# Optimization experiments

Hardware: AMD Instinct MI355X
Metric: run time of the kernel (lower is better)

The kernel has to match this reference:

```python
import jax, jax.numpy as jnp
import numpy as np

EPS = 1e-5
B, C, N = 2, 256, 65536


def conv1x1(x, W, b):
    # Conv1d with kernel_size=1: (B,Cin,N) x (Cout,Cin) -> (B,Cout,N)
    return jnp.einsum('oc,bcn->bon', W, x) + b[None, :, None]


def instance_norm(x):
    # InstanceNorm1d, affine=False, biased variance over the spatial dim
    m = jnp.mean(x, axis=-1, keepdims=True)
    v = jnp.var(x, axis=-1, keepdims=True)
    return (x - m) * jax.lax.rsqrt(v + EPS)


def mesh_conv(x, gemm, W, b):
    # MeshCNN MeshConv: gather self + 4 one-ring neighbor edges, symmetric fns, (1,5) conv.
    Bb, Cc, E = x.shape
    xp = jnp.concatenate([jnp.zeros((Bb, Cc, 1), x.dtype), x], axis=2)  # pad slot 0 (for -1/missing)
    eid = jnp.broadcast_to(jnp.arange(E, dtype=gemm.dtype)[None, :, None], (Bb, E, 1))
    Gi = jnp.concatenate([eid, gemm], axis=2) + 1                      # (B,E,5), +1 shift for pad row
    xt = xp.transpose(0, 2, 1)                                          # (B,E+1,C)
    f = jax.vmap(lambda xb, gb: xb[gb])(xt, Gi)                         # (B,E,5,C) gather
    f = f.transpose(0, 3, 1, 2)                                         # (B,C,E,5)
    f0, f1, f2, f3, f4 = (f[..., i] for i in range(5))
    g = jnp.stack([f0, f1 + f3, f2 + f4, jnp.abs(f1 - f3), jnp.abs(f2 - f4)], axis=-1)
    # Conv2d(Cin,Cout,(1,5)) over (B,C,E,5) -> (B,Cout,E)
    return jnp.einsum('ock,bcek->boe', W, g) + b[None, :, None]


def setup_inputs() -> dict:
    key = jax.random.key(0)
    ks = jax.random.split(key, 20)
    s = 0.05
    inp = {
        'x_0': jax.random.normal(ks[0], (B, C, N), jnp.float32),
        'x_1': jax.random.normal(ks[1], (B, C, N), jnp.float32),
        'gemm': jax.random.randint(ks[2], (B, N, 4), 0, N, jnp.int32),
        # conv_a / conv_b: C -> C//4
        'Wa': jax.random.normal(ks[3], (C // 4, C), jnp.float32) * s,
        'ba': jax.random.normal(ks[4], (C // 4,), jnp.float32) * s,
        'Wb': jax.random.normal(ks[5], (C // 4, C), jnp.float32) * s,
        'bb': jax.random.normal(ks[6], (C // 4,), jnp.float32) * s,
        # conv_a_local / conv_b_local: C//2 -> C//2
        'Wal': jax.random.normal(ks[7], (C // 2, C // 2), jnp.float32) * s,
        'bal': jax.random.normal(ks[8], (C // 2,), jnp.float32) * s,
        'Wbl': jax.random.normal(ks[9], (C // 2, C // 2), jnp.float32) * s,
        'bbl': jax.random.normal(ks[10], (C // 2,), jnp.float32) * s,
        # MeshConv weights: (Cout, Cin, 5)
        'Wat': jax.random.normal(ks[11], (C // 2, C // 2, 5), jnp.float32) * s,
        'bat': jax.random.normal(ks[12], (C // 2,), jnp.float32) * s,
        'Wbt': jax.random.normal(ks[13], (C // 2, C // 2, 5), jnp.float32) * s,
        'bbt': jax.random.normal(ks[14], (C // 2,), jnp.float32) * s,
        # fuse convs: C -> C
        'Waf': jax.random.normal(ks[15], (C, C), jnp.float32) * s,
        'baf': jax.random.normal(ks[16], (C,), jnp.float32) * s,
        'Wbf': jax.random.normal(ks[17], (C, C), jnp.float32) * s,
        'bbf': jax.random.normal(ks[18], (C,), jnp.float32) * s,
    }
    return inp


def reference(x_0, x_1, gemm, Wa, ba, Wb, bb, Wal, bal, Wbl, bbl,
              Wat, bat, Wbt, bbt, Waf, baf, Wbf, bbf):
    x_a = conv1x1(x_0, Wa, ba)
    x_b = conv1x1(x_1, Wb, bb)
    x_all = jnp.concatenate([x_a, x_b], axis=1)          # (B, C/2, N)
    a_local = conv1x1(x_all, Wal, bal)
    a_tri = mesh_conv(x_all, gemm, Wat, bat)
    x_a_two = jnp.concatenate([a_local, a_tri], axis=1)  # (B, C, N)
    b_local = conv1x1(x_all, Wbl, bbl)
    b_tri = mesh_conv(x_all, gemm, Wbt, bbt)
    x_b_two = jnp.concatenate([b_local, b_tri], axis=1)
    wa = jax.nn.sigmoid(instance_norm(conv1x1(x_a_two, Waf, baf)))
    wb = jax.nn.sigmoid(instance_norm(conv1x1(x_b_two, Wbf, bbf)))
    w = jax.nn.softmax(jnp.stack([wa, wb], axis=1), axis=1)  # (B,2,C,N)
    return x_0 * w[:, 0] + x_1 * w[:, 1]
```

## Files before the change

### kernel.cpp

```cpp
#include <hip/hip_runtime.h>
#include <stdint.h>

#define NEDGE 65536

typedef __attribute__((ext_vector_type(4))) float f32x4;
typedef __attribute__((ext_vector_type(8))) __bf16 bf16x8;

__device__ __forceinline__ uint16_t f2bf(float f) {
  union { float f; uint32_t u; } v; v.f = f;
  uint32_t r = v.u + 0x7FFFu + ((v.u >> 16) & 1u);
  return (uint16_t)(r >> 16);
}
__device__ __forceinline__ float bflo(uint32_t u) {
  union { uint32_t u; float f; } v; v.u = u << 16; return v.f;
}
__device__ __forceinline__ float bfhi(uint32_t u) {
  union { uint32_t u; float f; } v; v.u = u & 0xFFFF0000u; return v.f;
}
__device__ __forceinline__ uint32_t packbf(float lo, float hi) {
  return (uint32_t)f2bf(lo) | ((uint32_t)f2bf(hi) << 16);
}
__device__ __forceinline__ void gload_lds16(const void* g, void* l) {
  __builtin_amdgcn_global_load_lds(
      (__attribute__((address_space(1))) uint32_t*)(uintptr_t)g,
      (__attribute__((address_space(3))) uint32_t*)l, 16, 0, 0);
}
__device__ __forceinline__ float sigm(float z) { return 1.0f / (1.0f + __expf(-z)); }

__global__ void k_compose(const float* __restrict__ Wal, const float* __restrict__ Wbl,
                          const float* __restrict__ Wat, const float* __restrict__ Wbt,
                          const float* __restrict__ Waf, const float* __restrict__ Wbf,
                          uint16_t* __restrict__ Wt) {
  int id = blockIdx.x * 256 + threadIdx.x;
  if (id >= 512 * 640) return;
  int j = id / 640, kk = id % 640;
  const float* Wf = (j < 256) ? Waf : Wbf;
  const float* Wl = (j < 256) ? Wal : Wbl;
  const float* Wr = (j < 256) ? Wat : Wbt;
  int jj = j & 255;
  float acc = 0.f;
  if (kk < 128) {
    int c = kk;
    for (int o = 0; o < 128; ++o) acc += Wl[o * 128 + c] * Wf[jj * 256 + o];
    for (int o = 0; o < 128; ++o) acc += Wr[(o * 128 + c) * 5 + 0] * Wf[jj * 256 + 128 + o];
  } else {
    int blkid = (kk - 128) >> 7;
    int gk = (blkid == 0) ? 1 : (blkid == 1) ? 3 : (blkid == 2) ? 2 : 4;
    int c = (kk - 128) & 127;
    for (int o = 0; o < 128; ++o) acc += Wr[(o * 128 + c) * 5 + gk] * Wf[jj * 256 + 128 + o];
  }
  Wt[j * 640 + kk] = f2bf(acc);
}

__global__ void k_bias(const float* __restrict__ bal, const float* __restrict__ bat,
                       const float* __restrict__ baf, const float* __restrict__ bbl,
                       const float* __restrict__ bbt, const float* __restrict__ bbf,
                       const float* __restrict__ Waf, const float* __restrict__ Wbf,
                       float* __restrict__ biasF) {
  int id = blockIdx.x * 256 + threadIdx.x;
  if (id >= 512) return;
  const float* Wf = (id < 256) ? Waf : Wbf;
  const float* bl = (id < 256) ? bal : bbl;
  const float* bt = (id < 256) ? bat : bbt;
  const float* bsf = (id < 256) ? baf : bbf;
  int jj = id & 255;
  float acc = bsf[jj];
  for (int o = 0; o < 128; ++o) acc += Wf[jj * 256 + o] * bl[o];
  for (int o = 0; o < 128; ++o) acc += Wf[jj * 256 + 128 + o] * bt[o];
  biasF[id] = acc;
}

__global__ void k_wt1(const float* __restrict__ Wa, const float* __restrict__ Wb,
                      uint16_t* __restrict__ W1bf) {
  int id = blockIdx.x * 256 + threadIdx.x;
  if (id >= 2 * 64 * 256) return;
  int side = id >> 14, r = id & 16383;
  W1bf[id] = f2bf(side ? Wb[r] : Wa[r]);
}

__global__ __launch_bounds__(256) void k1_xa(
    const float* __restrict__ x0, const float* __restrict__ x1,
    const uint16_t* __restrict__ W1bf, const float* __restrict__ ba,
    const float* __restrict__ bb, uint16_t* __restrict__ XA) {
  __shared__ __align__(16) float Xs[2][32 * 128];
  __shared__ __align__(16) uint16_t Bs[64 * 256];
  int t = threadIdx.x;
  int side = blockIdx.y, b = blockIdx.z;
  int n0 = blockIdx.x * 128;
  const float* xin = (side ? x1 : x0) + (size_t)b * 256 * NEDGE + n0;
  const uint16_t* wsrc = W1bf + side * 64 * 256;

#pragma unroll
  for (int q = 0; q < 8; ++q) {
    int s = q * 256 + t;
    int j = s >> 5, pb = s & 31;
    int lb = pb ^ (j & 7);
    gload_lds16(wsrc + j * 256 + lb * 8, &Bs[s * 8]);
  }
#pragma unroll
  for (int q = 0; q < 4; ++q) {
    int s = q * 256 + t;
    int cl = s >> 5, pb = s & 31;
    int lb = pb ^ (((cl >> 3) & 3) << 2);
    gload_lds16(xin + (size_t)cl * NEDGE + lb * 4, &Xs[0][s * 4]);
  }

  int wv = t >> 6, l = t & 63;
  int m = l & 15, g = l >> 4;

  f32x4 acc[2][4];
  f32x4 zero = {0.f, 0.f, 0.f, 0.f};
#pragma unroll
  for (int rf = 0; rf < 2; ++rf)
#pragma unroll
    for (int cf = 0; cf < 4; ++cf) acc[rf][cf] = zero;

  for (int ks = 0; ks < 8; ++ks) {
    if (ks < 7) {
      const float* xc = xin + (size_t)(ks + 1) * 32 * NEDGE;
#pragma unroll
      for (int q = 0; q < 4; ++q) {
        int s = q * 256 + t;
        int cl = s >> 5, pb = s & 31;
        int lb = pb ^ (((cl >> 3) & 3) << 2);
        gload_lds16(xc + (size_t)cl * NEDGE + lb * 4, &Xs[(ks + 1) & 1][s * 4]);
      }
      asm volatile("s_waitcnt vmcnt(4)" ::: "memory");
    } else {
      asm volatile("s_waitcnt vmcnt(0)" ::: "memory");
    }
    __syncthreads();

    const float* Xb = Xs[ks & 1];
    bf16x8 bfr[4];
#pragma unroll
    for (int cf = 0; cf < 4; ++cf) {
      int jloc = cf * 16 + m;
      int pbb = (ks * 4 + g) ^ (jloc & 7);
      bfr[cf] = *(const bf16x8*)&Bs[jloc * 256 + pbb * 8];
    }
#pragma unroll
    for (int rf = 0; rf < 2; ++rf) {
      int nloc = rf * 64 + wv * 16 + m;
      int phys = (nloc >> 2) ^ (g << 2);
      const float* base = Xb + phys * 4 + (nloc & 3);
      float xv[8];
#pragma unroll
      for (int i = 0; i < 8; ++i) xv[i] = base[(g * 8 + i) * 128];
      union { bf16x8 v; __bf16 e[8]; } af;
#pragma unroll
      for (int i = 0; i < 8; ++i) af.e[i] = (__bf16)xv[i];
#pragma unroll
      for (int cf = 0; cf < 4; ++cf)
        acc[rf][cf] = __builtin_amdgcn_mfma_f32_16x16x32_bf16(af.v, bfr[cf], acc[rf][cf], 0, 0, 0);
    }
    __syncthreads();
  }

  const float* bias = side ? bb : ba;
  uint16_t* XAb = XA + ((size_t)b * NEDGE + n0) * 128 + side * 64;
#pragma unroll
  for (int rf = 0; rf < 2; ++rf)
#pragma unroll
    for (int cf = 0; cf < 4; ++cf) {
      float bv = bias[cf * 16 + m];
#pragma unroll
      for (int q = 0; q < 4; ++q) {
        int row = rf * 64 + wv * 16 + g * 4 + q;
        XAb[(size_t)row * 128 + cf * 16 + m] = f2bf(acc[rf][cf][q] + bv);
      }
    }
}

__device__ __forceinline__ void feat_pair(uint32_t u1, uint32_t u3, uint32_t& s, uint32_t& d) {
  float a1 = bflo(u1), b1 = bfhi(u1), a3 = bflo(u3), b3 = bfhi(u3);
  s = packbf(a1 + a3, b1 + b3);
  d = packbf(fabsf(a1 - a3), fabsf(b1 - b3));
}
__global__ void k2_gather(const uint16_t* __restrict__ XAb, const int* __restrict__ gidx,
                          uint16_t* __restrict__ G) {
  int t = threadIdx.x;
  int wid = t >> 6, lane = t & 63;
  int wbase = (blockIdx.x * 4 + wid) * 16;
  int g = lane >> 4, sl = lane & 15;
  for (int it = 0; it < 4; ++it) {
    int e0 = wbase + it * 4;
    int myidx = 0;
    if (lane < 16) myidx = gidx[(size_t)e0 * 4 + lane];
    int e = e0 + g;
    int i1 = __shfl(myidx, g * 4 + 0);
    int i2 = __shfl(myidx, g * 4 + 1);
    int i3 = __shfl(myidx, g * 4 + 2);
    int i4 = __shfl(myidx, g * 4 + 3);
    uint4 v1 = ((const uint4*)(XAb + (size_t)i1 * 128))[sl];
    uint4 v2 = ((const uint4*)(XAb + (size_t)i2 * 128))[sl];
    uint4 v3 = ((const uint4*)(XAb + (size_t)i3 * 128))[sl];
    uint4 v4 = ((const uint4*)(XAb + (size_t)i4 * 128))[sl];
    uint4 F1, F3, F2, F4;
    feat_pair(v1.x, v3.x, F1.x, F3.x); feat_pair(v1.y, v3.y, F1.y, F3.y);
    feat_pair(v1.z, v3.z, F1.z, F3.z); feat_pair(v1.w, v3.w, F1.w, F3.w);
    feat_pair(v2.x, v4.x, F2.x, F4.x); feat_pair(v2.y, v4.y, F2.y, F4.y);
    feat_pair(v2.z, v4.z, F2.z, F4.z); feat_pair(v2.w, v4.w, F2.w, F4.w);
    uint4* outr = (uint4*)(G + (size_t)e * 512);
    outr[sl] = F1; outr[16 + sl] = F3; outr[32 + sl] = F2; outr[48 + sl] = F4;
  }
}

__global__ __launch_bounds__(256, 2) void k3_gemm(
    const uint16_t* __restrict__ XAb, const uint16_t* __restrict__ G,
    const uint16_t* __restrict__ Wt, const float* __restrict__ biasF,
    uint16_t* __restrict__ Y) {
  __shared__ __align__(16) uint16_t As[128 * 64];
  __shared__ __align__(16) uint16_t Bs[128 * 64];
  int bx = blockIdx.y;
  int by = blockIdx.x;
  int t = threadIdx.x;
  int ebase = bx * 128;
  int jbase = by * 128;
  int wid = t >> 6, lane = t & 63;
  int wr = wid >> 1, wc = wid & 1;
  int m = lane & 15, half = lane >> 4;

  f32x4 acc[4][4];
  f32x4 zero = {0.f, 0.f, 0.f, 0.f};
#pragma unroll
  for (int r = 0; r < 4; ++r)
#pragma unroll
    for (int c = 0; c < 4; ++c) acc[r][c] = zero;

  for (int s = 0; s < 10; ++s) {
    const uint16_t* srcbase; size_t rstride; int koff;
    if (s < 2) { srcbase = XAb; rstride = 128; koff = s * 64; }
    else       { srcbase = G;   rstride = 512; koff = (s - 2) * 64; }
#pragma unroll
    for (int i = 0; i < 4; ++i) {
      int slot = i * 256 + t;
      int r = slot >> 3, c16 = slot & 7;
      gload_lds16(srcbase + (size_t)(ebase + r) * rstride + koff + c16 * 8, &As[slot * 8]);
    }
#pragma unroll
    for (int i = 0; i < 4; ++i) {
      int slot = i * 256 + t;
      int r = slot >> 3, c16 = slot & 7;
      gload_lds16(Wt + (size_t)(jbase + r) * 640 + s * 64 + c16 * 8, &Bs[slot * 8]);
    }
    asm volatile("s_waitcnt vmcnt(0)" ::: "memory");
    __syncthreads();
#pragma unroll
    for (int kit = 0; kit < 2; ++kit) {
      bf16x8 af[4], bf[4];
#pragma unroll
      for (int r = 0; r < 4; ++r) {
        int row = wr * 64 + r * 16 + m;
        af[r] = *(const bf16x8*)&As[row * 64 + kit * 32 + half * 8];
      }
#pragma unroll
      for (int cf = 0; cf < 4; ++cf) {
        int row = wc * 64 + cf * 16 + m;
        bf[cf] = *(const bf16x8*)&Bs[row * 64 + kit * 32 + half * 8];
      }
#pragma unroll
      for (int r = 0; r < 4; ++r)
#pragma unroll
        for (int cf = 0; cf < 4; ++cf)
          acc[r][cf] = __builtin_amdgcn_mfma_f32_16x16x32_bf16(af[r], bf[cf], acc[r][cf], 0, 0, 0);
    }
    __syncthreads();
  }
#pragma unroll
  for (int cf = 0; cf < 4; ++cf) {
    int col = jbase + wc * 64 + cf * 16 + m;
    float bv = biasF[col];
#pragma unroll
    for (int r = 0; r < 4; ++r) {
      int rowb = ebase + wr * 64 + r * 16 + half * 4;
#pragma unroll
      for (int q = 0; q < 4; ++q) {
        float v = acc[r][cf][q] + bv;
        Y[(size_t)(rowb + q) * 512 + col] = f2bf(v);
      }
    }
  }
}

__global__ void k3b1(const uint16_t* __restrict__ Y, float* __restrict__ part) {
  int t = threadIdx.x, ch = blockIdx.x;
  const uint32_t* Y32 = (const uint32_t*)Y;
  float s1a = 0, s2a = 0, s1b = 0, s2b = 0;
  size_t base = (size_t)ch * 128 * 256 + t;
  for (int r = 0; r < 128; ++r) {
    uint32_t v = Y32[base + (size_t)r * 256];
    float x = bflo(v), y = bfhi(v);
    s1a += x; s2a += x * x; s1b += y; s2b += y * y;
  }
  float* p = part + ((size_t)ch * 512 + 2 * t) * 2;
  p[0] = s1a; p[1] = s2a; p[2] = s1b; p[3] = s2b;
}
__global__ void k3b2(const float* __restrict__ part, float* __restrict__ statF) {
  int col = blockIdx.x, t = threadIdx.x;
  float s1 = 0, s2 = 0;
  for (int k = t; k < 512; k += 128) {
    const float* p = part + ((size_t)k * 512 + col) * 2;
    s1 += p[0]; s2 += p[1];
  }
  for (int off = 32; off; off >>= 1) { s1 += __shfl_down(s1, off); s2 += __shfl_down(s2, off); }
  __shared__ float sh[4];
  if ((t & 63) == 0) { sh[(t >> 6) * 2] = s1; sh[(t >> 6) * 2 + 1] = s2; }
  __syncthreads();
  if (t == 0) {
    s1 = sh[0] + sh[2]; s2 = sh[1] + sh[3];
    float mean = s1 * (1.0f / 65536.0f);
    float var = s2 * (1.0f / 65536.0f) - mean * mean;
    statF[col * 2] = mean;
    statF[col * 2 + 1] = rsqrtf(var + 1e-5f);
  }
}

__global__ __launch_bounds__(256) void k4_final(
    const uint16_t* __restrict__ Y, const float* __restrict__ statF,
    const float* __restrict__ x0b, const float* __restrict__ x1b,
    float* __restrict__ outb) {
  __shared__ float W0[128][65];
  __shared__ float mA[128], rA[128], mB[128], rB[128];
  int t = threadIdx.x;
  int n0 = blockIdx.x * 64;
  int ch = blockIdx.y;
  if (t < 128) {
    mA[t] = statF[(ch * 128 + t) * 2];
    rA[t] = statF[(ch * 128 + t) * 2 + 1];
  } else {
    int q = t - 128;
    mB[q] = statF[(256 + ch * 128 + q) * 2];
    rB[q] = statF[(256 + ch * 128 + q) * 2 + 1];
  }
  __syncthreads();
  const char* Ybase = (const char*)Y;
  for (int i = t; i < 64 * 64; i += 256) {
    int row = i >> 6, cp = i & 63;
    const char* yr = Ybase + (size_t)(n0 + row) * 1024;
    uint32_t ya2 = *(const uint32_t*)(yr + ch * 256 + cp * 4);
    uint32_t yb2 = *(const uint32_t*)(yr + 512 + ch * 256 + cp * 4);
    int c0 = 2 * cp, c1 = 2 * cp + 1;
    float wa0 = sigm((bflo(ya2) - mA[c0]) * rA[c0]);
    float wa1 = sigm((bfhi(ya2) - mA[c1]) * rA[c1]);
    float wb0 = sigm((bflo(yb2) - mB[c0]) * rB[c0]);
    float wb1 = sigm((bfhi(yb2) - mB[c1]) * rB[c1]);
    W0[c0][row] = sigm(wa0 - wb0);
    W0[c1][row] = sigm(wa1 - wb1);
  }
  __syncthreads();
  int nn = t & 63, cg = t >> 6;
  for (int cc = cg; cc < 128; cc += 4) {
    int c = ch * 128 + cc;
    size_t gi = (size_t)c * NEDGE + n0 + nn;
    float w0 = W0[cc][nn];
    outb[gi] = x0b[gi] * w0 + x1b[gi] * (1.0f - w0);
  }
}

extern "C" void kernel_launch(void* const* d_in, const int* in_sizes, int n_in,
                              void* d_out, int out_size, void* d_ws, size_t ws_size,
                              hipStream_t stream) {
  const float* x0 = (const float*)d_in[0];
  const float* x1 = (const float*)d_in[1];
  const int* gemm = (const int*)d_in[2];
  const float* Wa = (const float*)d_in[3];
  const float* ba = (const float*)d_in[4];
  const float* Wb = (const float*)d_in[5];
  const float* bb = (const float*)d_in[6];
  const float* Wal = (const float*)d_in[7];
  const float* bal = (const float*)d_in[8];
  const float* Wbl = (const float*)d_in[9];
  const float* bbl = (const float*)d_in[10];
  const float* Wat = (const float*)d_in[11];
  const float* bat = (const float*)d_in[12];
  const float* Wbt = (const float*)d_in[13];
  const float* bbt = (const float*)d_in[14];
  const float* Waf = (const float*)d_in[15];
  const float* baf = (const float*)d_in[16];
  const float* Wbf = (const float*)d_in[17];
  const float* bbf = (const float*)d_in[18];
  float* out = (float*)d_out;

  char* ws = (char*)d_ws;
  uint16_t* XA   = (uint16_t*)ws;
  uint16_t* G    = (uint16_t*)(ws + 33554432);
  uint16_t* Yb   = (uint16_t*)(ws + 100663296);
  uint16_t* Wt   = (uint16_t*)(ws + 167772160);
  uint16_t* W1bf = (uint16_t*)(ws + 168427520);
  float*    biasF= (float*)(ws + 168558592);
  float*    part = (float*)(ws + 168560640);
  float*    statF= (float*)(ws + 170657792);

  k_compose<<<dim3(1280), dim3(256), 0, stream>>>(Wal, Wbl, Wat, Wbt, Waf, Wbf, Wt);
  k_bias<<<dim3(2), dim3(256), 0, stream>>>(bal, bat, baf, bbl, bbt, bbf, Waf, Wbf, biasF);
  k_wt1<<<dim3(128), dim3(256), 0, stream>>>(Wa, Wb, W1bf);
  k1_xa<<<dim3(512, 2, 2), dim3(256), 0, stream>>>(x0, x1, W1bf, ba, bb, XA);

  for (int b = 0; b < 2; ++b) {
    const uint16_t* XAb = XA + (size_t)b * NEDGE * 128;
    k2_gather<<<dim3(1024), dim3(256), 0, stream>>>(XAb, gemm + (size_t)b * NEDGE * 4, G);
    k3_gemm<<<dim3(4, 512), dim3(256), 0, stream>>>(XAb, G, Wt, biasF, Yb);
    k3b1<<<dim3(512), dim3(256), 0, stream>>>(Yb, part);
    k3b2<<<dim3(512), dim3(128), 0, stream>>>(part, statF + b * 1024);
    k4_final<<<dim3(1024, 2), dim3(256), 0, stream>>>(
        Yb, statF + b * 1024, x0 + (size_t)b * 256 * NEDGE,
        x1 + (size_t)b * 256 * NEDGE, out + (size_t)b * 256 * NEDGE);
  }
}
```

Measured before the change: 434.8 us.

## Triple-buffer k1 input loads and double-buffer k3 GEMM with swizzled LDS

k1 now keeps three LDS input stages so global loads run two K-steps ahead, and switches to raw s_barrier with sched_barrier to control the waits. k3 gains double-buffered A/B tiles, issuing the next stage's global-to-LDS loads before computing the current one, and XOR-swizzles LDS columns to cut bank conflicts on the MFMA operand reads. Both changes target load latency stalls and LDS conflicts in the main GEMMs. In exchange, LDS use per block rises, which may lower occupancy, particularly for k3 with launch bounds of 2 blocks.

```diff
diff --git a/kernel.cpp b/kernel.cpp
--- a/kernel.cpp
+++ b/kernel.cpp
@@ -82,7 +82,7 @@
     const float* __restrict__ x0, const float* __restrict__ x1,
     const uint16_t* __restrict__ W1bf, const float* __restrict__ ba,
     const float* __restrict__ bb, uint16_t* __restrict__ XA) {
-  __shared__ __align__(16) float Xs[2][32 * 128];
+  __shared__ __align__(16) float Xs[3][32 * 128];
   __shared__ __align__(16) uint16_t Bs[64 * 256];
   int t = threadIdx.x;
   int side = blockIdx.y, b = blockIdx.z;
@@ -98,11 +98,14 @@
     gload_lds16(wsrc + j * 256 + lb * 8, &Bs[s * 8]);
   }
 #pragma unroll
-  for (int q = 0; q < 4; ++q) {
-    int s = q * 256 + t;
-    int cl = s >> 5, pb = s & 31;
-    int lb = pb ^ (((cl >> 3) & 3) << 2);
-    gload_lds16(xin + (size_t)cl * NEDGE + lb * 4, &Xs[0][s * 4]);
+  for (int c = 0; c < 2; ++c) {
+#pragma unroll
+    for (int q = 0; q < 4; ++q) {
+      int s = q * 256 + t;
+      int cl = s >> 5, pb = s & 31;
+      int lb = pb ^ (((cl >> 3) & 3) << 2);
+      gload_lds16(xin + (size_t)(c * 32 + cl) * NEDGE + lb * 4, &Xs[c][s * 4]);
+    }
   }
 
   int wv = t >> 6, l = t & 63;
@@ -115,23 +118,27 @@
 #pragma unroll
     for (int cf = 0; cf < 4; ++cf) acc[rf][cf] = zero;
 
+#pragma unroll
   for (int ks = 0; ks < 8; ++ks) {
-    if (ks < 7) {
-      const float* xc = xin + (size_t)(ks + 1) * 32 * NEDGE;
+    if (ks < 6) {
+      const float* xc = xin + (size_t)(ks + 2) * 32 * NEDGE;
 #pragma unroll
       for (int q = 0; q < 4; ++q) {
         int s = q * 256 + t;
         int cl = s >> 5, pb = s & 31;
         int lb = pb ^ (((cl >> 3) & 3) << 2);
-        gload_lds16(xc + (size_t)cl * NEDGE + lb * 4, &Xs[(ks + 1) & 1][s * 4]);
+        gload_lds16(xc + (size_t)cl * NEDGE + lb * 4, &Xs[(ks + 2) % 3][s * 4]);
       }
+      asm volatile("s_waitcnt vmcnt(8)" ::: "memory");
+    } else if (ks == 6) {
       asm volatile("s_waitcnt vmcnt(4)" ::: "memory");
     } else {
       asm volatile("s_waitcnt vmcnt(0)" ::: "memory");
     }
-    __syncthreads();
-
-    const float* Xb = Xs[ks & 1];
+    __builtin_amdgcn_sched_barrier(0);
+    __builtin_amdgcn_s_barrier();
+
+    const float* Xb = Xs[ks % 3];
     bf16x8 bfr[4];
 #pragma unroll
     for (int cf = 0; cf < 4; ++cf) {
@@ -154,7 +161,7 @@
       for (int cf = 0; cf < 4; ++cf)
         acc[rf][cf] = __builtin_amdgcn_mfma_f32_16x16x32_bf16(af.v, bfr[cf], acc[rf][cf], 0, 0, 0);
     }
-    __syncthreads();
+    __builtin_amdgcn_s_barrier();
   }
 
   const float* bias = side ? bb : ba;
@@ -210,8 +217,8 @@
     const uint16_t* __restrict__ XAb, const uint16_t* __restrict__ G,
     const uint16_t* __restrict__ Wt, const float* __restrict__ biasF,
     uint16_t* __restrict__ Y) {
-  __shared__ __align__(16) uint16_t As[128 * 64];
-  __shared__ __align__(16) uint16_t Bs[128 * 64];
+  __shared__ __align__(16) uint16_t As[2][128 * 64];
+  __shared__ __align__(16) uint16_t Bs2[2][128 * 64];
   int bx = blockIdx.y;
   int by = blockIdx.x;
   int t = threadIdx.x;
@@ -228,36 +235,52 @@
 #pragma unroll
     for (int c = 0; c < 4; ++c) acc[r][c] = zero;
 
+#define K3_STAGE(s_, bi)                                                        \
+  do {                                                                          \
+    const uint16_t* srcb; size_t rstr; int koff;                                \
+    if ((s_) < 2) { srcb = XAb; rstr = 128; koff = (s_) * 64; }                 \
+    else          { srcb = G;   rstr = 512; koff = ((s_) - 2) * 64; }           \
+    _Pragma("unroll")                                                           \
+    for (int i = 0; i < 4; ++i) {                                               \
+      int slot = i * 256 + t; int r = slot >> 3, c16 = slot & 7;                \
+      gload_lds16(srcb + (size_t)(ebase + r) * rstr + koff + (c16 ^ (r & 7)) * 8, \
+                  &As[bi][slot * 8]);                                           \
+    }                                                                           \
+    _Pragma("unroll")                                                           \
+    for (int i = 0; i < 4; ++i) {                                               \
+      int slot = i * 256 + t; int r = slot >> 3, c16 = slot & 7;                \
+      gload_lds16(Wt + (size_t)(jbase + r) * 640 + (s_) * 64 + (c16 ^ (r & 7)) * 8, \
+                  &Bs2[bi][slot * 8]);                                          \
+    }                                                                           \
+  } while (0)
+
+  K3_STAGE(0, 0);
+
+#pragma unroll
   for (int s = 0; s < 10; ++s) {
-    const uint16_t* srcbase; size_t rstride; int koff;
-    if (s < 2) { srcbase = XAb; rstride = 128; koff = s * 64; }
-    else       { srcbase = G;   rstride = 512; koff = (s - 2) * 64; }
-#pragma unroll
-    for (int i = 0; i < 4; ++i) {
-      int slot = i * 256 + t;
-      int r = slot >> 3, c16 = slot & 7;
-      gload_lds16(srcbase + (size_t)(ebase + r) * rstride + koff + c16 * 8, &As[slot * 8]);
-    }
-#pragma unroll
-    for (int i = 0; i < 4; ++i) {
-      int slot = i * 256 + t;
-      int r = slot >> 3, c16 = slot & 7;
-      gload_lds16(Wt + (size_t)(jbase + r) * 640 + s * 64 + c16 * 8, &Bs[slot * 8]);
-    }
-    asm volatile("s_waitcnt vmcnt(0)" ::: "memory");
-    __syncthreads();
+    if (s < 9) {
+      K3_STAGE(s + 1, (s + 1) & 1);
+      asm volatile("s_waitcnt vmcnt(8)" ::: "memory");
+    } else {
+      asm volatile("s_waitcnt vmcnt(0)" ::: "memory");
+    }
+    __builtin_amdgcn_sched_barrier(0);
+    __builtin_amdgcn_s_barrier();
+
+    const uint16_t* Ab = As[s & 1];
+    const uint16_t* Bb = Bs2[s & 1];
 #pragma unroll
     for (int kit = 0; kit < 2; ++kit) {
       bf16x8 af[4], bf[4];
 #pragma unroll
       for (int r = 0; r < 4; ++r) {
         int row = wr * 64 + r * 16 + m;
-        af[r] = *(const bf16x8*)&As[row * 64 + kit * 32 + half * 8];
+        af[r] = *(const bf16x8*)&Ab[row * 64 + ((kit * 4 + half) ^ (m & 7)) * 8];
       }
 #pragma unroll
       for (int cf = 0; cf < 4; ++cf) {
         int row = wc * 64 + cf * 16 + m;
-        bf[cf] = *(const bf16x8*)&Bs[row * 64 + kit * 32 + half * 8];
+        bf[cf] = *(const bf16x8*)&Bb[row * 64 + ((kit * 4 + half) ^ (m & 7)) * 8];
       }
 #pragma unroll
       for (int r = 0; r < 4; ++r)
@@ -265,8 +288,10 @@
         for (int cf = 0; cf < 4; ++cf)
           acc[r][cf] = __builtin_amdgcn_mfma_f32_16x16x32_bf16(af[r], bf[cf], acc[r][cf], 0, 0, 0);
     }
-    __syncthreads();
-  }
+    __builtin_amdgcn_s_barrier();
+  }
+#undef K3_STAGE
+
 #pragma unroll
   for (int cf = 0; cf < 4; ++cf) {
     int col = jbase + wc * 64 + cf * 16 + m;
```

Result: no change. 428.9 us (-1.3%).
